# Kernel optimization log

Measured on AMD Instinct MI355X. Metric: run time of the kernel, lower is better.

The kernel has to match this reference:

```python
import jax, jax.numpy as jnp
import numpy as np

C = jnp.complex64
NQ = 4  # qubits per register (module-level `qubits` constant)

_CNOT = jnp.array([[1,0,0,0],[0,1,0,0],[0,0,0,1],[0,0,1,0]], dtype=C)
_X = jnp.array([[0,1],[1,0]], dtype=C)

def _RZ(t):
    e = jnp.exp((-0.5j) * t.astype(C))
    z = jnp.zeros((), C)
    return jnp.stack([jnp.stack([e, z]), jnp.stack([z, jnp.conj(e)])])

def _RX(t):
    c = jnp.cos(0.5 * t).astype(C)
    s = (-1j) * jnp.sin(0.5 * t).astype(C)
    return jnp.stack([jnp.stack([c, s]), jnp.stack([s, c])])

def _CRX(t):
    return jnp.eye(4, dtype=C).at[2:, 2:].set(_RX(t))

def _IXX(t):
    c = jnp.cos(0.5 * t).astype(C)
    s = (-1j) * jnp.sin(0.5 * t).astype(C)
    return c * jnp.eye(4, dtype=C) + s * jnp.fliplr(jnp.eye(4, dtype=C))

def _ap1(psi, U, w):
    psi = jnp.moveaxis(psi, w, 0)
    psi = jnp.tensordot(U, psi, axes=([1], [0]))
    return jnp.moveaxis(psi, 0, w)

def _ap2(psi, U, w1, w2):
    psi = jnp.moveaxis(psi, (w1, w2), (0, 1))
    shp = psi.shape
    psi = (U @ psi.reshape(4, -1)).reshape(shp)
    return jnp.moveaxis(psi, (0, 1), (w1, w2))

def _expZ(psi, w):
    p = psi.real ** 2 + psi.imag ** 2
    p = jnp.moveaxis(p, w, 0).reshape(2, -1).sum(axis=1)
    return p[0] - p[1]

def _expX(psi, w):
    return jnp.real(jnp.vdot(psi, _ap1(psi, _X, w)))

def _init_state(n):
    return jnp.zeros((2,) * n, C).at[(0,) * n].set(1.0 + 0.0j)

def _rot_layer(psi, rot, offset, start):
    for i in range(NQ):
        idx = start + 3 * i
        w = offset + i
        psi = _ap1(psi, _RZ(rot[idx]), w)
        psi = _ap1(psi, _RX(rot[idx + 1]), w)
        psi = _ap1(psi, _RZ(rot[idx + 2]), w)
    return psi

def _two_ring(psi, rot, crx, offset):
    # depth == 2 (24 rot params): one rot layer before entanglers, one after.
    psi = _rot_layer(psi, rot, offset, 0)
    for i in range(NQ):
        psi = _ap2(psi, _CRX(crx[i]), offset + i, offset + (i + 1) % NQ)
    for i in range(NQ):  # len(crx)==2*NQ -> IsingXX ring
        psi = _ap2(psi, _IXX(crx[NQ + i]), offset + i, offset + (i + 1) % NQ)
    psi = _rot_layer(psi, rot, offset, 3 * NQ)
    return psi

def _score_circuit(xq, xk, wq_rot, wq_crx, wk_rot, wk_crx, wc_rot, wc_crx, wc_crx2):
    psi = _init_state(2 * NQ)
    for i in range(NQ):  # AngleEmbedding (default rotation='X')
        psi = _ap1(psi, _RX(xq[i]), i)
    psi = _two_ring(psi, wq_rot, wq_crx, 0)
    for i in range(NQ):
        psi = _ap1(psi, _RX(xk[i]), NQ + i)
    psi = _two_ring(psi, wk_rot, wk_crx, NQ)
    for i in range(NQ):
        psi = _ap2(psi, _CRX(wc_crx[i]), i, i + NQ)
        psi = _ap2(psi, _CRX(wc_crx[i + NQ]), i + NQ, i)
    for i in range(NQ):
        psi = _ap2(psi, _CRX(wc_crx2[i]), i, (i + 1) % NQ + NQ)
    for i in range(NQ):
        psi = _ap2(psi, _CRX(wc_crx2[i + NQ]), i + NQ, (i + 1) % NQ)
    for i in range(NQ):
        psi = _ap2(psi, _CNOT, i, i + NQ)
        psi = _ap2(psi, _CNOT, i + NQ, i)
    psi = _rot_layer(psi, wc_rot, 0, 0)
    z = jnp.stack([_expZ(psi, w) for w in range(NQ)])
    x = jnp.stack([_expX(psi, w) for w in range(NQ)])
    return jnp.concatenate([z, x])

def _value_circuit(xv, amp, wv_rot, wv_crx, gates):
    psi = _init_state(NQ)
    for i in range(NQ):
        psi = _ap1(psi, _RX(xv[i]), i)
    psi = _two_ring(psi, wv_rot, wv_crx, 0)
    for i in range(NQ):
        psi = _ap1(psi, _RX(jnp.tanh(amp[i]) * gates[i]), i)
    for i in range(NQ):
        psi = _ap2(psi, _CNOT, i, (i + 1) % NQ)
    z = jnp.stack([_expZ(psi, w) for w in range(NQ)])
    x = jnp.stack([_expX(psi, w) for w in range(NQ)])
    return jnp.concatenate([z, x])

def setup_inputs() -> dict:
    key = jax.random.key(0)
    ks = jax.random.split(key, 16)
    B, IN = 4096, 96
    hp = np.pi / 2
    return {
        'x_text': jax.random.normal(ks[0], (B, IN), jnp.float32),
        'x_image': jax.random.normal(ks[1], (B, IN), jnp.float32),
        'W_text': jax.random.normal(ks[2], (NQ, IN), jnp.float32) * 0.1,
        'b_text': jnp.zeros((NQ,), jnp.float32),
        'W_image': jax.random.normal(ks[3], (NQ, IN), jnp.float32) * 0.1,
        'b_image': jnp.zeros((NQ,), jnp.float32),
        'weights_q_rot': jax.random.uniform(ks[4], (6 * NQ,), jnp.float32, -hp, hp),
        'weights_q_crx': jax.random.normal(ks[5], (2 * NQ,), jnp.float32) * 0.1,
        'weights_k_rot': jax.random.uniform(ks[6], (6 * NQ,), jnp.float32, -hp, hp),
        'weights_k_crx': jax.random.normal(ks[7], (2 * NQ,), jnp.float32) * 0.1,
        'weights_v_rot': jax.random.uniform(ks[8], (6 * NQ,), jnp.float32, -hp, hp),
        'weights_v_crx': jax.random.normal(ks[9], (2 * NQ,), jnp.float32) * 0.1,
        'weights_cross_rot': jax.random.uniform(ks[10], (3 * NQ,), jnp.float32, -hp, hp),
        'weights_cross_crx': jax.random.normal(ks[11], (2 * NQ,), jnp.float32) * 0.1,
        'weights_cross_crx2': jax.random.normal(ks[12], (2 * NQ,), jnp.float32) * 0.1,
        'score_gates': jnp.full((NQ,), np.pi, jnp.float32),
    }

def reference(x_text, x_image, W_text, b_text, W_image, b_image,
              weights_q_rot, weights_q_crx, weights_k_rot, weights_k_crx,
              weights_v_rot, weights_v_crx, weights_cross_rot,
              weights_cross_crx, weights_cross_crx2, score_gates):
    # anneal alpha = 1.0 and all QAFConfig flags True -> effective params = raw params
    xq = x_text @ W_text.T + b_text   # [B, 4]
    xk = x_image @ W_image.T + b_image
    score = jax.vmap(lambda a, b: _score_circuit(
        a, b, weights_q_rot, weights_q_crx, weights_k_rot, weights_k_crx,
        weights_cross_rot, weights_cross_crx, weights_cross_crx2))(xq, xk)  # [B, 8]
    amp = jnp.sqrt(score[:, :NQ] ** 2 + score[:, NQ:] ** 2)  # [B, 4]
    out = jax.vmap(lambda v, a: _value_circuit(
        v, a, weights_v_rot, weights_v_crx, score_gates))(xk, amp)  # [B, 8]
    return out.astype(jnp.float32)
```

## Files before the change

### kernel.cpp

```cpp
#include <hip/hip_runtime.h>
#include <math.h>

#define DEV __device__ __forceinline__

template<int M>
DEV float lxor(float x) {
    const int i = __builtin_bit_cast(int, x);
    int r;
    if constexpr (M == 1)      r = __builtin_amdgcn_update_dpp(i, i, 0xB1, 0xF, 0xF, false);
    else if constexpr (M == 2) r = __builtin_amdgcn_update_dpp(i, i, 0x4E, 0xF, 0xF, false);
    else if constexpr (M == 3) r = __builtin_amdgcn_update_dpp(i, i, 0x1B, 0xF, 0xF, false);
    else if constexpr (M == 8) r = __builtin_amdgcn_update_dpp(i, i, 0x128, 0xF, 0xF, false);
    else                       r = __builtin_amdgcn_ds_swizzle(i, (M << 10) | 0x1F);
    return __builtin_bit_cast(float, r);
}
template<int M> DEV float2 lxor2(float2 v) {
    return make_float2(lxor<M>(v.x), lxor<M>(v.y));
}
DEV float red16(float x) {
    x += lxor<8>(x); x += lxor<4>(x); x += lxor<2>(x); x += lxor<1>(x);
    return x;
}

template<int LM>
DEV void sgate(float2& v, int l16, float2 u00, float2 u01) {
    const bool hi = (l16 & LM) != 0;
    const float e00x = u00.x, e00y = hi ? -u00.y : u00.y;
    const float e01x = hi ? -u01.x : u01.x, e01y = u01.y;
    const float2 p = lxor2<LM>(v);
    v = make_float2(e00x*v.x - e00y*v.y + e01x*p.x - e01y*p.y,
                    e00x*v.y + e00y*v.x + e01x*p.y + e01y*p.x);
}
template<int LM>
DEV void sgate4(float2& v, int l16, float4 g) {
    sgate<LM>(v, l16, make_float2(g.x, g.y), make_float2(g.z, g.w));
}
template<int CL, int LM>
DEV void scrx(float2& v, int l16, float2 cs) {
    const bool hi = (l16 & CL) != 0;
    const float c = hi ? cs.x : 1.f, sn = hi ? cs.y : 0.f;
    const float2 p = lxor2<LM>(v);
    v = make_float2(c*v.x + sn*p.y, c*v.y - sn*p.x);
}
template<int LM2>
DEV void sixx(float2& v, float2 cs) {
    const float2 p = lxor2<LM2>(v);
    v = make_float2(cs.x*v.x + cs.y*p.y, cs.x*v.y - cs.y*p.x);
}
template<int LM>
DEV void srx(float2& v, float c, float sn) {
    const float2 p = lxor2<LM>(v);
    v = make_float2(c*v.x + sn*p.y, c*v.y - sn*p.x);
}
template<int CL, int LM>
DEV void scnot(float2& v, int l16) {
    const float2 p = lxor2<LM>(v);
    const bool hi = (l16 & CL) != 0;
    v = hi ? p : v;
}

template<int CM, int LM>
DEV void crx_rl(float2 (&s)[16], float2 cs) {
#pragma unroll
    for (int r = 0; r < 16; r++) {
        if (!(r & CM)) continue;
        const float2 p = lxor2<LM>(s[r]);
        const float2 a = s[r];
        s[r] = make_float2(cs.x*a.x + cs.y*p.y, cs.x*a.y - cs.y*p.x);
    }
}
template<int CL, int TM>
DEV void crx_lr(float2 (&s)[16], int l16, float2 cs) {
    const bool hi = (l16 & CL) != 0;
    const float c = hi ? cs.x : 1.f, sn = hi ? cs.y : 0.f;
#pragma unroll
    for (int r = 0; r < 16; r++) {
        if (r & TM) continue;
        const int r1 = r | TM;
        const float2 a = s[r], b = s[r1];
        s[r]  = make_float2(c*a.x + sn*b.y, c*a.y - sn*b.x);
        s[r1] = make_float2(c*b.x + sn*a.y, c*b.y - sn*a.x);
    }
}
template<int CM, int LM>
DEV void cnot_rl(float2 (&s)[16]) {
#pragma unroll
    for (int r = 0; r < 16; r++) {
        if (r & CM) s[r] = lxor2<LM>(s[r]);
    }
}
template<int CL, int TM>
DEV void cnot_lr(float2 (&s)[16], int l16) {
    const bool hi = (l16 & CL) != 0;
#pragma unroll
    for (int r = 0; r < 16; r++) {
        if (r & TM) continue;
        const int r1 = r | TM;
        const float2 a = s[r], b = s[r1];
        s[r]  = hi ? b : a;
        s[r1] = hi ? a : b;
    }
}

template<int RM>
DEV void measU(const float2 (&s)[16], const float (&n2)[16],
               float4 mz, float2 bx, float& z, float& x) {
    float zz = 0.f, xx = 0.f;
#pragma unroll
    for (int r = 0; r < 16; r++) {
        if (r & RM) continue;
        const int r1 = r | RM;
        const float nd  = n2[r] - n2[r1];
        const float dre = s[r].x*s[r1].x + s[r].y*s[r1].y;
        const float dim = s[r].x*s[r1].y - s[r].y*s[r1].x;
        zz += mz.x*nd + mz.y*dre - mz.z*dim;
        xx += mz.w*nd + bx.x*dre - bx.y*dim;
    }
    z = zz; x = xx;
}

DEV void fuse_rx(float4 g, float ang, float2& u00, float2& u01) {
    float s_, c_;
    __sincosf(0.5f * ang, &s_, &c_);
    u00 = make_float2(g.x*c_ + g.w*s_, g.y*c_ - g.z*s_);
    u01 = make_float2(g.y*s_ + g.z*c_, -g.x*s_ + g.w*c_);
}

__global__ __launch_bounds__(256, 1) void qa_kernel(
    const float* __restrict__ x_text, const float* __restrict__ x_image,
    const float* __restrict__ W_text, const float* __restrict__ b_text,
    const float* __restrict__ W_image, const float* __restrict__ b_image,
    const float* __restrict__ wq_rot, const float* __restrict__ wq_crx,
    const float* __restrict__ wk_rot, const float* __restrict__ wk_crx,
    const float* __restrict__ wv_rot, const float* __restrict__ wv_crx,
    const float* __restrict__ wc_rot, const float* __restrict__ wc_crx,
    const float* __restrict__ wc_crx2, const float* __restrict__ gates,
    float* __restrict__ out, int B)
{
    __shared__ float4 sG[28];
    __shared__ float2 sCS[40];
    __shared__ float4 sWT[192];
    __shared__ float4 sMZ[4];
    __shared__ float2 sBX[4];
    __shared__ __align__(16) float2 sQ[16][18];

    const int tid = threadIdx.x;
    if (tid < 192) {
        const float* W = (tid < 96) ? W_text : W_image;
        const int idx = (tid < 96) ? tid : tid - 96;
        sWT[tid] = make_float4(W[idx], W[96 + idx], W[192 + idx], W[288 + idx]);
    }
    if (tid < 28) {
        const float* srcs[7] = {wq_rot, wq_rot + 12, wk_rot, wk_rot + 12,
                                wc_rot, wv_rot, wv_rot + 12};
        const float* p = srcs[tid >> 2] + 3 * (tid & 3);
        const float a = p[0], bb = p[1], c = p[2];
        float sh, ch, sd, cd, sb, cb;
        __sincosf(0.5f * (a + c), &sh, &ch);
        __sincosf(0.5f * (a - c), &sd, &cd);
        __sincosf(0.5f * bb, &sb, &cb);
        const float4 g = make_float4(cb * ch, -cb * sh, sb * sd, -sb * cd);
        sG[tid] = g;
        if (tid >= 16 && tid < 20) {
            const int w = tid - 16;
            const float2 u00 = make_float2(g.x, g.y), u01 = make_float2(g.z, g.w);
            const float az = u00.x*u00.x + u00.y*u00.y - u01.x*u01.x - u01.y*u01.y;
            sMZ[w] = make_float4(az,
                                 4.f*(u00.x*u01.x + u00.y*u01.y),
                                 4.f*(u00.x*u01.y - u00.y*u01.x),
                                 -2.f*(u00.x*u01.x - u00.y*u01.y));
            sBX[w] = make_float2(
                2.f*(u00.x*u00.x - u00.y*u00.y - u01.x*u01.x + u01.y*u01.y),
                -4.f*(u00.x*u00.y + u01.x*u01.y));
        }
    }
    if (tid < 40) {
        const float* srcs[5] = {wq_crx, wk_crx, wc_crx, wc_crx2, wv_crx};
        const float t = srcs[tid >> 3][tid & 7];
        float s_, c_;
        __sincosf(0.5f * t, &s_, &c_);
        sCS[tid] = make_float2(c_, s_);
    }
    __syncthreads();

    const int l16 = tid & 15;
    const int elem = tid >> 4;
    const int b = blockIdx.x * 16 + elem;

    const float* xt = x_text + (size_t)b * 96;
    const float* xi = x_image + (size_t)b * 96;
    float aq[4] = {0.f, 0.f, 0.f, 0.f}, ak[4] = {0.f, 0.f, 0.f, 0.f};
#pragma unroll
    for (int kk = 0; kk < 6; kk++) {
        const int idx = l16 + 16 * kk;
        const float vq = xt[idx], vk = xi[idx];
        const float4 wq = sWT[idx], wk = sWT[96 + idx];
        aq[0] += vq * wq.x; aq[1] += vq * wq.y; aq[2] += vq * wq.z; aq[3] += vq * wq.w;
        ak[0] += vk * wk.x; ak[1] += vk * wk.y; ak[2] += vk * wk.z; ak[3] += vk * wk.w;
    }
    float xq[4], xk[4];
#pragma unroll
    for (int j = 0; j < 4; j++) {
        xq[j] = red16(aq[j]) + b_text[j];
        xk[j] = red16(ak[j]) + b_image[j];
    }

    float2 q  = make_float2((l16 == 0) ? 1.f : 0.f, 0.f);
    float2 k  = q, vv = q;
    {
        float2 u00, u01;
        fuse_rx(sG[0],  xq[0], u00, u01); sgate<8>(q,  l16, u00, u01);
        fuse_rx(sG[8],  xk[0], u00, u01); sgate<8>(k,  l16, u00, u01);
        fuse_rx(sG[20], xk[0], u00, u01); sgate<8>(vv, l16, u00, u01);
        fuse_rx(sG[1],  xq[1], u00, u01); sgate<4>(q,  l16, u00, u01);
        fuse_rx(sG[9],  xk[1], u00, u01); sgate<4>(k,  l16, u00, u01);
        fuse_rx(sG[21], xk[1], u00, u01); sgate<4>(vv, l16, u00, u01);
        fuse_rx(sG[2],  xq[2], u00, u01); sgate<2>(q,  l16, u00, u01);
        fuse_rx(sG[10], xk[2], u00, u01); sgate<2>(k,  l16, u00, u01);
        fuse_rx(sG[22], xk[2], u00, u01); sgate<2>(vv, l16, u00, u01);
        fuse_rx(sG[3],  xq[3], u00, u01); sgate<1>(q,  l16, u00, u01);
        fuse_rx(sG[11], xk[3], u00, u01); sgate<1>(k,  l16, u00, u01);
        fuse_rx(sG[23], xk[3], u00, u01); sgate<1>(vv, l16, u00, u01);
    }
    scrx<8, 4>(q, l16, sCS[0]);  scrx<8, 4>(k, l16, sCS[8]);  scrx<8, 4>(vv, l16, sCS[32]);
    scrx<4, 2>(q, l16, sCS[1]);  scrx<4, 2>(k, l16, sCS[9]);  scrx<4, 2>(vv, l16, sCS[33]);
    scrx<2, 1>(q, l16, sCS[2]);  scrx<2, 1>(k, l16, sCS[10]); scrx<2, 1>(vv, l16, sCS[34]);
    scrx<1, 8>(q, l16, sCS[3]);  scrx<1, 8>(k, l16, sCS[11]); scrx<1, 8>(vv, l16, sCS[35]);
    sixx<12>(q, sCS[4]);  sixx<12>(k, sCS[12]); sixx<12>(vv, sCS[36]);
    sixx<6>(q, sCS[5]);   sixx<6>(k, sCS[13]);  sixx<6>(vv, sCS[37]);
    sixx<3>(q, sCS[6]);   sixx<3>(k, sCS[14]);  sixx<3>(vv, sCS[38]);
    sixx<9>(q, sCS[7]);   sixx<9>(k, sCS[15]);  sixx<9>(vv, sCS[39]);
    sgate4<8>(q, l16, sG[4]);  sgate4<8>(k, l16, sG[12]);  sgate4<8>(vv, l16, sG[24]);
    sgate4<4>(q, l16, sG[5]);  sgate4<4>(k, l16, sG[13]);  sgate4<4>(vv, l16, sG[25]);
    sgate4<2>(q, l16, sG[6]);  sgate4<2>(k, l16, sG[14]);  sgate4<2>(vv, l16, sG[26]);
    sgate4<1>(q, l16, sG[7]);  sgate4<1>(k, l16, sG[15]);  sgate4<1>(vv, l16, sG[27]);

    sQ[elem][l16] = q;
    const float4* qrow = reinterpret_cast<const float4*>(&sQ[elem][0]);
    float2 s[16];
#pragma unroll
    for (int j = 0; j < 8; j++) {
        const float4 t = qrow[j];
        s[2*j]   = make_float2(t.x*k.x - t.y*k.y, t.x*k.y + t.y*k.x);
        s[2*j+1] = make_float2(t.z*k.x - t.w*k.y, t.z*k.y + t.w*k.x);
    }

    crx_rl<8, 8>(s, sCS[16]); crx_lr<8, 8>(s, l16, sCS[20]);
    crx_rl<4, 4>(s, sCS[17]); crx_lr<4, 4>(s, l16, sCS[21]);
    crx_rl<2, 2>(s, sCS[18]); crx_lr<2, 2>(s, l16, sCS[22]);
    crx_rl<1, 1>(s, sCS[19]); crx_lr<1, 1>(s, l16, sCS[23]);
    crx_rl<8, 4>(s, sCS[24]); crx_rl<4, 2>(s, sCS[25]);
    crx_rl<2, 1>(s, sCS[26]); crx_rl<1, 8>(s, sCS[27]);
    crx_lr<8, 4>(s, l16, sCS[28]); crx_lr<4, 2>(s, l16, sCS[29]);
    crx_lr<2, 1>(s, l16, sCS[30]); crx_lr<1, 8>(s, l16, sCS[31]);
    cnot_rl<8, 8>(s); cnot_lr<8, 8>(s, l16);
    cnot_rl<4, 4>(s); cnot_lr<4, 4>(s, l16);
    cnot_rl<2, 2>(s); cnot_lr<2, 2>(s, l16);
    cnot_rl<1, 1>(s); cnot_lr<1, 1>(s, l16);

    float n2[16];
#pragma unroll
    for (int r = 0; r < 16; r++) n2[r] = s[r].x*s[r].x + s[r].y*s[r].y;
    float amp[4];
    {
        float z0, x0, z1, x1, z2, x2, z3, x3;
        measU<8>(s, n2, sMZ[0], sBX[0], z0, x0);
        measU<4>(s, n2, sMZ[1], sBX[1], z1, x1);
        measU<2>(s, n2, sMZ[2], sBX[2], z2, x2);
        measU<1>(s, n2, sMZ[3], sBX[3], z3, x3);
        z0 = red16(z0); x0 = red16(x0);
        z1 = red16(z1); x1 = red16(x1);
        z2 = red16(z2); x2 = red16(x2);
        z3 = red16(z3); x3 = red16(x3);
        amp[0] = sqrtf(z0*z0 + x0*x0);
        amp[1] = sqrtf(z1*z1 + x1*x1);
        amp[2] = sqrtf(z2*z2 + x2*x2);
        amp[3] = sqrtf(z3*z3 + x3*x3);
    }

#pragma unroll
    for (int i = 0; i < 4; i++) {
        const float e = __expf(2.f * amp[i]);
        const float th = 1.f - 2.f / (e + 1.f);
        const float ang = th * gates[i];
        float s_, c_;
        __sincosf(0.5f * ang, &s_, &c_);
        if (i == 0) srx<8>(vv, c_, s_);
        if (i == 1) srx<4>(vv, c_, s_);
        if (i == 2) srx<2>(vv, c_, s_);
        if (i == 3) srx<1>(vv, c_, s_);
    }
    scnot<8, 4>(vv, l16); scnot<4, 2>(vv, l16);
    scnot<2, 1>(vv, l16); scnot<1, 8>(vv, l16);

    const float vn2 = vv.x*vv.x + vv.y*vv.y;
    float oz[4], ox[4];
    {
        const float2 p8 = lxor2<8>(vv), p4 = lxor2<4>(vv),
                     p2 = lxor2<2>(vv), p1 = lxor2<1>(vv);
        oz[0] = red16((l16 & 8) ? -vn2 : vn2);
        oz[1] = red16((l16 & 4) ? -vn2 : vn2);
        oz[2] = red16((l16 & 2) ? -vn2 : vn2);
        oz[3] = red16((l16 & 1) ? -vn2 : vn2);
        ox[0] = red16(vv.x*p8.x + vv.y*p8.y);
        ox[1] = red16(vv.x*p4.x + vv.y*p4.y);
        ox[2] = red16(vv.x*p2.x + vv.y*p2.y);
        ox[3] = red16(vv.x*p1.x + vv.y*p1.y);
    }
    if (l16 == 0) {
        float4* o = (float4*)(out + (size_t)b * 8);
        o[0] = make_float4(oz[0], oz[1], oz[2], oz[3]);
        o[1] = make_float4(ox[0], ox[1], ox[2], ox[3]);
    }
}

extern "C" void kernel_launch(void* const* d_in, const int* in_sizes, int n_in,
                              void* d_out, int out_size, void* d_ws, size_t ws_size,
                              hipStream_t stream) {
    (void)n_in; (void)out_size; (void)d_ws; (void)ws_size;
    const int B = in_sizes[0] / 96;
    const dim3 grid((B + 15) / 16), block(256);
    hipLaunchKernelGGL(qa_kernel, grid, block, 0, stream,
                       (const float*)d_in[0], (const float*)d_in[1],
                       (const float*)d_in[2], (const float*)d_in[3],
                       (const float*)d_in[4], (const float*)d_in[5],
                       (const float*)d_in[6], (const float*)d_in[7],
                       (const float*)d_in[8], (const float*)d_in[9],
                       (const float*)d_in[10], (const float*)d_in[11],
                       (const float*)d_in[12], (const float*)d_in[13],
                       (const float*)d_in[14], (const float*)d_in[15],
                       (float*)d_out, B);
}
```

Measured before the change: 93.28 us.

## Split each batch element's 8-qubit state across 32 lanes instead of 16

Each batch element now uses 32 lanes, so every lane holds 8 amplitudes instead of 16. The Q and K 4-qubit registers are evolved in the two half-warps in parallel rather than serially in one lane group. Qubit gates on the new lane bit use cross-lane swizzles (lxor<16>), and the reductions widen to 32 lanes. The register footprint per lane is halved and the launch-bounds occupancy hint is raised to 2. In exchange the grid doubles, the V circuit is computed redundantly in both halves, and there is extra cross-lane shuffle traffic.

```diff
diff --git a/kernel.cpp b/kernel.cpp
--- a/kernel.cpp
+++ b/kernel.cpp
@@ -21,6 +21,10 @@
     x += lxor<8>(x); x += lxor<4>(x); x += lxor<2>(x); x += lxor<1>(x);
     return x;
 }
+DEV float red32(float x) {
+    x += lxor<16>(x);
+    return red16(x);
+}
 
 template<int LM>
 DEV void sgate(float2& v, int l16, float2 u00, float2 u01) {
@@ -60,54 +64,73 @@
 }
 
 template<int CM, int LM>
-DEV void crx_rl(float2 (&s)[16], float2 cs) {
-#pragma unroll
-    for (int r = 0; r < 16; r++) {
+DEV void fcrx_rl(float2 (&s)[8], float2 cs) {
+#pragma unroll
+    for (int r = 0; r < 8; r++) {
         if (!(r & CM)) continue;
         const float2 p = lxor2<LM>(s[r]);
         const float2 a = s[r];
         s[r] = make_float2(cs.x*a.x + cs.y*p.y, cs.x*a.y - cs.y*p.x);
     }
 }
-template<int CL, int TM>
-DEV void crx_lr(float2 (&s)[16], int l16, float2 cs) {
-    const bool hi = (l16 & CL) != 0;
+template<int CL, int RM>
+DEV void fcrx_lr(float2 (&s)[8], int l32, float2 cs) {
+    const bool hi = (l32 & CL) != 0;
     const float c = hi ? cs.x : 1.f, sn = hi ? cs.y : 0.f;
 #pragma unroll
-    for (int r = 0; r < 16; r++) {
-        if (r & TM) continue;
-        const int r1 = r | TM;
+    for (int r = 0; r < 8; r++) {
+        if (r & RM) continue;
+        const int r1 = r | RM;
         const float2 a = s[r], b = s[r1];
         s[r]  = make_float2(c*a.x + sn*b.y, c*a.y - sn*b.x);
         s[r1] = make_float2(c*b.x + sn*a.y, c*b.y - sn*a.x);
     }
 }
+template<int CL, int LM>
+DEV void fcrx_ll(float2 (&s)[8], int l32, float2 cs) {
+    const bool hi = (l32 & CL) != 0;
+    const float c = hi ? cs.x : 1.f, sn = hi ? cs.y : 0.f;
+#pragma unroll
+    for (int r = 0; r < 8; r++) {
+        const float2 p = lxor2<LM>(s[r]);
+        const float2 a = s[r];
+        s[r] = make_float2(c*a.x + sn*p.y, c*a.y - sn*p.x);
+    }
+}
 template<int CM, int LM>
-DEV void cnot_rl(float2 (&s)[16]) {
-#pragma unroll
-    for (int r = 0; r < 16; r++) {
+DEV void fcnot_rl(float2 (&s)[8]) {
+#pragma unroll
+    for (int r = 0; r < 8; r++)
         if (r & CM) s[r] = lxor2<LM>(s[r]);
-    }
-}
-template<int CL, int TM>
-DEV void cnot_lr(float2 (&s)[16], int l16) {
-    const bool hi = (l16 & CL) != 0;
-#pragma unroll
-    for (int r = 0; r < 16; r++) {
-        if (r & TM) continue;
-        const int r1 = r | TM;
+}
+template<int CL, int RM>
+DEV void fcnot_lr(float2 (&s)[8], int l32) {
+    const bool hi = (l32 & CL) != 0;
+#pragma unroll
+    for (int r = 0; r < 8; r++) {
+        if (r & RM) continue;
+        const int r1 = r | RM;
         const float2 a = s[r], b = s[r1];
         s[r]  = hi ? b : a;
         s[r1] = hi ? a : b;
     }
 }
+template<int CL, int LM>
+DEV void fcnot_ll(float2 (&s)[8], int l32) {
+    const bool hi = (l32 & CL) != 0;
+#pragma unroll
+    for (int r = 0; r < 8; r++) {
+        const float2 p = lxor2<LM>(s[r]);
+        s[r] = hi ? p : s[r];
+    }
+}
 
 template<int RM>
-DEV void measU(const float2 (&s)[16], const float (&n2)[16],
+DEV void measR(const float2 (&s)[8], const float (&n2)[8],
                float4 mz, float2 bx, float& z, float& x) {
     float zz = 0.f, xx = 0.f;
 #pragma unroll
-    for (int r = 0; r < 16; r++) {
+    for (int r = 0; r < 8; r++) {
         if (r & RM) continue;
         const int r1 = r | RM;
         const float nd  = n2[r] - n2[r1];
@@ -118,6 +141,21 @@
     }
     z = zz; x = xx;
 }
+DEV void measL16(const float2 (&s)[8], const float (&n2)[8], int l32,
+                 float4 mz, float2 bx, float& z, float& x) {
+    const float f = (l32 & 16) ? -1.f : 1.f;
+    float zz = 0.f, xx = 0.f;
+#pragma unroll
+    for (int r = 0; r < 8; r++) {
+        const float2 p = lxor2<16>(s[r]);
+        const float tre = s[r].x*p.x + s[r].y*p.y;
+        const float ftim = f * (s[r].x*p.y - s[r].y*p.x);
+        const float fn = f * n2[r];
+        zz += mz.x*fn + 0.5f*(mz.y*tre - mz.z*ftim);
+        xx += mz.w*fn + 0.5f*(bx.x*tre - bx.y*ftim);
+    }
+    z = zz; x = xx;
+}
 
 DEV void fuse_rx(float4 g, float ang, float2& u00, float2& u01) {
     float s_, c_;
@@ -126,7 +164,7 @@
     u01 = make_float2(g.y*s_ + g.z*c_, -g.x*s_ + g.w*c_);
 }
 
-__global__ __launch_bounds__(256, 1) void qa_kernel(
+__global__ __launch_bounds__(256, 2) void qa_kernel(
     const float* __restrict__ x_text, const float* __restrict__ x_image,
     const float* __restrict__ W_text, const float* __restrict__ b_text,
     const float* __restrict__ W_image, const float* __restrict__ b_image,
@@ -142,7 +180,7 @@
     __shared__ float4 sWT[192];
     __shared__ float4 sMZ[4];
     __shared__ float2 sBX[4];
-    __shared__ __align__(16) float2 sQ[16][18];
+    __shared__ __align__(16) float2 sQK[8][32];
 
     const int tid = threadIdx.x;
     if (tid < 192) {
@@ -183,16 +221,18 @@
     }
     __syncthreads();
 
+    const int l32 = tid & 31;
     const int l16 = tid & 15;
-    const int elem = tid >> 4;
-    const int b = blockIdx.x * 16 + elem;
+    const int hi = (l32 >> 4) & 1;
+    const int elem = tid >> 5;
+    const int b = blockIdx.x * 8 + elem;
 
     const float* xt = x_text + (size_t)b * 96;
     const float* xi = x_image + (size_t)b * 96;
     float aq[4] = {0.f, 0.f, 0.f, 0.f}, ak[4] = {0.f, 0.f, 0.f, 0.f};
 #pragma unroll
-    for (int kk = 0; kk < 6; kk++) {
-        const int idx = l16 + 16 * kk;
+    for (int kk = 0; kk < 3; kk++) {
+        const int idx = l32 + 32 * kk;
         const float vq = xt[idx], vk = xi[idx];
         const float4 wq = sWT[idx], wk = sWT[96 + idx];
         aq[0] += vq * wq.x; aq[1] += vq * wq.y; aq[2] += vq * wq.z; aq[3] += vq * wq.w;
@@ -201,77 +241,81 @@
     float xq[4], xk[4];
 #pragma unroll
     for (int j = 0; j < 4; j++) {
-        xq[j] = red16(aq[j]) + b_text[j];
-        xk[j] = red16(ak[j]) + b_image[j];
-    }
-
-    float2 q  = make_float2((l16 == 0) ? 1.f : 0.f, 0.f);
-    float2 k  = q, vv = q;
+        xq[j] = red32(aq[j]) + b_text[j];
+        xk[j] = red32(ak[j]) + b_image[j];
+    }
+
+    const float4* gA = sG + (hi ? 8 : 0);
+    const float2* cA = sCS + (hi ? 8 : 0);
+    float2 A = make_float2((l16 == 0) ? 1.f : 0.f, 0.f);
+    float2 V = A;
     {
         float2 u00, u01;
-        fuse_rx(sG[0],  xq[0], u00, u01); sgate<8>(q,  l16, u00, u01);
-        fuse_rx(sG[8],  xk[0], u00, u01); sgate<8>(k,  l16, u00, u01);
-        fuse_rx(sG[20], xk[0], u00, u01); sgate<8>(vv, l16, u00, u01);
-        fuse_rx(sG[1],  xq[1], u00, u01); sgate<4>(q,  l16, u00, u01);
-        fuse_rx(sG[9],  xk[1], u00, u01); sgate<4>(k,  l16, u00, u01);
-        fuse_rx(sG[21], xk[1], u00, u01); sgate<4>(vv, l16, u00, u01);
-        fuse_rx(sG[2],  xq[2], u00, u01); sgate<2>(q,  l16, u00, u01);
-        fuse_rx(sG[10], xk[2], u00, u01); sgate<2>(k,  l16, u00, u01);
-        fuse_rx(sG[22], xk[2], u00, u01); sgate<2>(vv, l16, u00, u01);
-        fuse_rx(sG[3],  xq[3], u00, u01); sgate<1>(q,  l16, u00, u01);
-        fuse_rx(sG[11], xk[3], u00, u01); sgate<1>(k,  l16, u00, u01);
-        fuse_rx(sG[23], xk[3], u00, u01); sgate<1>(vv, l16, u00, u01);
-    }
-    scrx<8, 4>(q, l16, sCS[0]);  scrx<8, 4>(k, l16, sCS[8]);  scrx<8, 4>(vv, l16, sCS[32]);
-    scrx<4, 2>(q, l16, sCS[1]);  scrx<4, 2>(k, l16, sCS[9]);  scrx<4, 2>(vv, l16, sCS[33]);
-    scrx<2, 1>(q, l16, sCS[2]);  scrx<2, 1>(k, l16, sCS[10]); scrx<2, 1>(vv, l16, sCS[34]);
-    scrx<1, 8>(q, l16, sCS[3]);  scrx<1, 8>(k, l16, sCS[11]); scrx<1, 8>(vv, l16, sCS[35]);
-    sixx<12>(q, sCS[4]);  sixx<12>(k, sCS[12]); sixx<12>(vv, sCS[36]);
-    sixx<6>(q, sCS[5]);   sixx<6>(k, sCS[13]);  sixx<6>(vv, sCS[37]);
-    sixx<3>(q, sCS[6]);   sixx<3>(k, sCS[14]);  sixx<3>(vv, sCS[38]);
-    sixx<9>(q, sCS[7]);   sixx<9>(k, sCS[15]);  sixx<9>(vv, sCS[39]);
-    sgate4<8>(q, l16, sG[4]);  sgate4<8>(k, l16, sG[12]);  sgate4<8>(vv, l16, sG[24]);
-    sgate4<4>(q, l16, sG[5]);  sgate4<4>(k, l16, sG[13]);  sgate4<4>(vv, l16, sG[25]);
-    sgate4<2>(q, l16, sG[6]);  sgate4<2>(k, l16, sG[14]);  sgate4<2>(vv, l16, sG[26]);
-    sgate4<1>(q, l16, sG[7]);  sgate4<1>(k, l16, sG[15]);  sgate4<1>(vv, l16, sG[27]);
-
-    sQ[elem][l16] = q;
-    const float4* qrow = reinterpret_cast<const float4*>(&sQ[elem][0]);
-    float2 s[16];
-#pragma unroll
-    for (int j = 0; j < 8; j++) {
+        fuse_rx(gA[0], hi ? xk[0] : xq[0], u00, u01); sgate<8>(A, l16, u00, u01);
+        fuse_rx(sG[20], xk[0], u00, u01);             sgate<8>(V, l16, u00, u01);
+        fuse_rx(gA[1], hi ? xk[1] : xq[1], u00, u01); sgate<4>(A, l16, u00, u01);
+        fuse_rx(sG[21], xk[1], u00, u01);             sgate<4>(V, l16, u00, u01);
+        fuse_rx(gA[2], hi ? xk[2] : xq[2], u00, u01); sgate<2>(A, l16, u00, u01);
+        fuse_rx(sG[22], xk[2], u00, u01);             sgate<2>(V, l16, u00, u01);
+        fuse_rx(gA[3], hi ? xk[3] : xq[3], u00, u01); sgate<1>(A, l16, u00, u01);
+        fuse_rx(sG[23], xk[3], u00, u01);             sgate<1>(V, l16, u00, u01);
+    }
+    scrx<8, 4>(A, l16, cA[0]);  scrx<8, 4>(V, l16, sCS[32]);
+    scrx<4, 2>(A, l16, cA[1]);  scrx<4, 2>(V, l16, sCS[33]);
+    scrx<2, 1>(A, l16, cA[2]);  scrx<2, 1>(V, l16, sCS[34]);
+    scrx<1, 8>(A, l16, cA[3]);  scrx<1, 8>(V, l16, sCS[35]);
+    sixx<12>(A, cA[4]);  sixx<12>(V, sCS[36]);
+    sixx<6>(A, cA[5]);   sixx<6>(V, sCS[37]);
+    sixx<3>(A, cA[6]);   sixx<3>(V, sCS[38]);
+    sixx<9>(A, cA[7]);   sixx<9>(V, sCS[39]);
+    sgate4<8>(A, l16, gA[4]);  sgate4<8>(V, l16, sG[24]);
+    sgate4<4>(A, l16, gA[5]);  sgate4<4>(V, l16, sG[25]);
+    sgate4<2>(A, l16, gA[6]);  sgate4<2>(V, l16, sG[26]);
+    sgate4<1>(A, l16, gA[7]);  sgate4<1>(V, l16, sG[27]);
+
+    sQK[elem][(hi << 4) | l16] = A;
+    asm volatile("" ::: "memory");
+    const float2 kk2 = sQK[elem][16 + l16];
+    const float4* qrow = reinterpret_cast<const float4*>(&sQK[elem][hi << 3]);
+    float2 s[8];
+#pragma unroll
+    for (int j = 0; j < 4; j++) {
         const float4 t = qrow[j];
-        s[2*j]   = make_float2(t.x*k.x - t.y*k.y, t.x*k.y + t.y*k.x);
-        s[2*j+1] = make_float2(t.z*k.x - t.w*k.y, t.z*k.y + t.w*k.x);
-    }
-
-    crx_rl<8, 8>(s, sCS[16]); crx_lr<8, 8>(s, l16, sCS[20]);
-    crx_rl<4, 4>(s, sCS[17]); crx_lr<4, 4>(s, l16, sCS[21]);
-    crx_rl<2, 2>(s, sCS[18]); crx_lr<2, 2>(s, l16, sCS[22]);
-    crx_rl<1, 1>(s, sCS[19]); crx_lr<1, 1>(s, l16, sCS[23]);
-    crx_rl<8, 4>(s, sCS[24]); crx_rl<4, 2>(s, sCS[25]);
-    crx_rl<2, 1>(s, sCS[26]); crx_rl<1, 8>(s, sCS[27]);
-    crx_lr<8, 4>(s, l16, sCS[28]); crx_lr<4, 2>(s, l16, sCS[29]);
-    crx_lr<2, 1>(s, l16, sCS[30]); crx_lr<1, 8>(s, l16, sCS[31]);
-    cnot_rl<8, 8>(s); cnot_lr<8, 8>(s, l16);
-    cnot_rl<4, 4>(s); cnot_lr<4, 4>(s, l16);
-    cnot_rl<2, 2>(s); cnot_lr<2, 2>(s, l16);
-    cnot_rl<1, 1>(s); cnot_lr<1, 1>(s, l16);
-
-    float n2[16];
-#pragma unroll
-    for (int r = 0; r < 16; r++) n2[r] = s[r].x*s[r].x + s[r].y*s[r].y;
+        s[2*j]   = make_float2(t.x*kk2.x - t.y*kk2.y, t.x*kk2.y + t.y*kk2.x);
+        s[2*j+1] = make_float2(t.z*kk2.x - t.w*kk2.y, t.z*kk2.y + t.w*kk2.x);
+    }
+
+    fcrx_ll<16, 8>(s, l32, sCS[16]); fcrx_ll<8, 16>(s, l32, sCS[20]);
+    fcrx_rl<4, 4>(s, sCS[17]);       fcrx_lr<4, 4>(s, l32, sCS[21]);
+    fcrx_rl<2, 2>(s, sCS[18]);       fcrx_lr<2, 2>(s, l32, sCS[22]);
+    fcrx_rl<1, 1>(s, sCS[19]);       fcrx_lr<1, 1>(s, l32, sCS[23]);
+    fcrx_ll<16, 4>(s, l32, sCS[24]);
+    fcrx_rl<4, 2>(s, sCS[25]);
+    fcrx_rl<2, 1>(s, sCS[26]);
+    fcrx_rl<1, 8>(s, sCS[27]);
+    fcrx_lr<8, 4>(s, l32, sCS[28]);
+    fcrx_lr<4, 2>(s, l32, sCS[29]);
+    fcrx_lr<2, 1>(s, l32, sCS[30]);
+    fcrx_ll<1, 16>(s, l32, sCS[31]);
+    fcnot_ll<16, 8>(s, l32); fcnot_ll<8, 16>(s, l32);
+    fcnot_rl<4, 4>(s);       fcnot_lr<4, 4>(s, l32);
+    fcnot_rl<2, 2>(s);       fcnot_lr<2, 2>(s, l32);
+    fcnot_rl<1, 1>(s);       fcnot_lr<1, 1>(s, l32);
+
+    float n2[8];
+#pragma unroll
+    for (int r = 0; r < 8; r++) n2[r] = s[r].x*s[r].x + s[r].y*s[r].y;
     float amp[4];
     {
         float z0, x0, z1, x1, z2, x2, z3, x3;
-        measU<8>(s, n2, sMZ[0], sBX[0], z0, x0);
-        measU<4>(s, n2, sMZ[1], sBX[1], z1, x1);
-        measU<2>(s, n2, sMZ[2], sBX[2], z2, x2);
-        measU<1>(s, n2, sMZ[3], sBX[3], z3, x3);
-        z0 = red16(z0); x0 = red16(x0);
-        z1 = red16(z1); x1 = red16(x1);
-        z2 = red16(z2); x2 = red16(x2);
-        z3 = red16(z3); x3 = red16(x3);
+        measL16(s, n2, l32, sMZ[0], sBX[0], z0, x0);
+        measR<4>(s, n2, sMZ[1], sBX[1], z1, x1);
+        measR<2>(s, n2, sMZ[2], sBX[2], z2, x2);
+        measR<1>(s, n2, sMZ[3], sBX[3], z3, x3);
+        z0 = red32(z0); x0 = red32(x0);
+        z1 = red32(z1); x1 = red32(x1);
+        z2 = red32(z2); x2 = red32(x2);
+        z3 = red32(z3); x3 = red32(x3);
         amp[0] = sqrtf(z0*z0 + x0*x0);
         amp[1] = sqrtf(z1*z1 + x1*x1);
         amp[2] = sqrtf(z2*z2 + x2*x2);
@@ -285,29 +329,29 @@
         const float ang = th * gates[i];
         float s_, c_;
         __sincosf(0.5f * ang, &s_, &c_);
-        if (i == 0) srx<8>(vv, c_, s_);
-        if (i == 1) srx<4>(vv, c_, s_);
-        if (i == 2) srx<2>(vv, c_, s_);
-        if (i == 3) srx<1>(vv, c_, s_);
-    }
-    scnot<8, 4>(vv, l16); scnot<4, 2>(vv, l16);
-    scnot<2, 1>(vv, l16); scnot<1, 8>(vv, l16);
-
-    const float vn2 = vv.x*vv.x + vv.y*vv.y;
+        if (i == 0) srx<8>(V, c_, s_);
+        if (i == 1) srx<4>(V, c_, s_);
+        if (i == 2) srx<2>(V, c_, s_);
+        if (i == 3) srx<1>(V, c_, s_);
+    }
+    scnot<8, 4>(V, l16); scnot<4, 2>(V, l16);
+    scnot<2, 1>(V, l16); scnot<1, 8>(V, l16);
+
+    const float vn2 = V.x*V.x + V.y*V.y;
     float oz[4], ox[4];
     {
-        const float2 p8 = lxor2<8>(vv), p4 = lxor2<4>(vv),
-                     p2 = lxor2<2>(vv), p1 = lxor2<1>(vv);
+        const float2 p8 = lxor2<8>(V), p4 = lxor2<4>(V),
+                     p2 = lxor2<2>(V), p1 = lxor2<1>(V);
         oz[0] = red16((l16 & 8) ? -vn2 : vn2);
         oz[1] = red16((l16 & 4) ? -vn2 : vn2);
         oz[2] = red16((l16 & 2) ? -vn2 : vn2);
         oz[3] = red16((l16 & 1) ? -vn2 : vn2);
-        ox[0] = red16(vv.x*p8.x + vv.y*p8.y);
-        ox[1] = red16(vv.x*p4.x + vv.y*p4.y);
-        ox[2] = red16(vv.x*p2.x + vv.y*p2.y);
-        ox[3] = red16(vv.x*p1.x + vv.y*p1.y);
-    }
-    if (l16 == 0) {
+        ox[0] = red16(V.x*p8.x + V.y*p8.y);
+        ox[1] = red16(V.x*p4.x + V.y*p4.y);
+        ox[2] = red16(V.x*p2.x + V.y*p2.y);
+        ox[3] = red16(V.x*p1.x + V.y*p1.y);
+    }
+    if (l32 == 0) {
         float4* o = (float4*)(out + (size_t)b * 8);
         o[0] = make_float4(oz[0], oz[1], oz[2], oz[3]);
         o[1] = make_float4(ox[0], ox[1], ox[2], ox[3]);
@@ -319,7 +363,7 @@
                               hipStream_t stream) {
     (void)n_in; (void)out_size; (void)d_ws; (void)ws_size;
     const int B = in_sizes[0] / 96;
-    const dim3 grid((B + 15) / 16), block(256);
+    const dim3 grid((B + 7) / 8), block(256);
     hipLaunchKernelGGL(qa_kernel, grid, block, 0, stream,
                        (const float*)d_in[0], (const float*)d_in[1],
                        (const float*)d_in[2], (const float*)d_in[3],
```

Measured after the change: 91.82 us. About the same (-1.6%).
